# Kernel optimization log

Hardware: AMD Instinct MI355X
Metric: run time of the kernel (lower is better)

Reference implementation:

```python
import jax, jax.numpy as jnp
import numpy as np

N, E, NNZ = 50000, 10000, 250000   # nodes, hyperedges, incidences
IN_CH, H, D = 128, 64, 6           # in_channels, MLP_hidden, stalk dim
EPS = 1e-5


def setup_inputs() -> dict:
    key = jax.random.key(0)
    ks = jax.random.split(key, 12)
    inp = {}
    inp["x"] = jax.random.normal(ks[0], (N, IN_CH), jnp.float32)
    inp["hyperedge_attr"] = jax.random.normal(ks[1], (E, IN_CH), jnp.float32)  # init_hedge='rand'
    inp["node_idx"] = jax.random.randint(ks[2], (NNZ,), 0, N)
    inp["edge_idx"] = jax.random.randint(ks[3], (NNZ,), 0, E)
    inp["node_types"] = jax.random.randint(ks[4], (N,), 0, 3)
    inp["hyperedge_types"] = jax.random.randint(ks[5], (E,), 0, 6)
    s = 1.0 / np.sqrt(IN_CH)
    inp["W_lin"] = jax.random.uniform(ks[6], (IN_CH, H * D), jnp.float32, -s, s)
    inp["b_lin"] = jnp.zeros((H * D,), jnp.float32)
    inp["ln_g"] = jnp.ones((2 * H,), jnp.float32)
    inp["ln_b"] = jnp.zeros((2 * H,), jnp.float32)
    s2 = 1.0 / np.sqrt(2 * H)
    inp["W_sheaf"] = jax.random.uniform(ks[7], (2 * H, D), jnp.float32, -s2, s2)
    inp["b_sheaf"] = jnp.zeros((D,), jnp.float32)
    s3 = 1.0 / np.sqrt(H)
    inp["W_conv0"] = jax.random.uniform(ks[8], (H, H), jnp.float32, -s3, s3)
    inp["b_conv0"] = jnp.zeros((H,), jnp.float32)
    inp["W_conv1"] = jax.random.uniform(ks[9], (H, H), jnp.float32, -s3, s3)
    inp["b_conv1"] = jnp.zeros((H,), jnp.float32)
    return inp


def _layernorm(x, g, b):
    mu = x.mean(-1, keepdims=True)
    var = ((x - mu) ** 2).mean(-1, keepdims=True)
    return (x - mu) * jax.lax.rsqrt(var + EPS) * g + b


def reference(x, hyperedge_attr, node_idx, edge_idx, node_types, hyperedge_types,
              W_lin, b_lin, ln_g, ln_b, W_sheaf, b_sheaf,
              W_conv0, b_conv0, W_conv1, b_conv1):
    # --- input projection + stalk reshape (self.lin) ---
    xs = (x @ W_lin + b_lin).reshape(N * D, H)              # [N*d, H]
    es = (hyperedge_attr @ W_lin + b_lin).reshape(E * D, H)  # [E*d, H]

    # --- SheafBuilderDiag (local_concat, sigmoid act) ---
    xa = xs.reshape(N, D, H).mean(1)   # [N, H] stalk-averaged node feats
    ea = es.reshape(E, D, H).mean(1)   # [E, H]
    feat = jnp.concatenate([xa[node_idx], ea[edge_idx]], axis=-1)  # [NNZ, 2H]
    alpha = jax.nn.sigmoid(_layernorm(feat, ln_g, ln_b) @ W_sheaf + b_sheaf)  # [NNZ, D]

    dr = jnp.arange(D)
    row_exp = (node_idx[:, None] * D + dr).reshape(-1)  # [NNZ*D] expanded node index
    col_exp = (edge_idx[:, None] * D + dr).reshape(-1)  # [NNZ*D] expanded hyperedge index
    a = alpha.reshape(-1)                               # [NNZ*D]

    # --- degree_norm: D^-1 (nodes) and B^-1 (hyperedges) from incidence counts ---
    ones = jnp.ones_like(a)
    Dn = jax.ops.segment_sum(ones, row_exp, num_segments=N * D)
    Dinv = jnp.where(Dn > 0, 1.0 / Dn, 0.0)
    Bn = jax.ops.segment_sum(ones, col_exp, num_segments=E * D)
    Binv = jnp.where(Bn > 0, 1.0 / Bn, 0.0)

    def conv(xin, W, bias):
        # HyperDiffusionDiagSheafConv: out = xW - D^-1 H^T B^-1 H (xW) + bias
        xl = xin @ W
        m = Binv[:, None] * jax.ops.segment_sum(a[:, None] * xl[row_exp], col_exp, num_segments=E * D)
        agg = Dinv[:, None] * jax.ops.segment_sum(a[:, None] * m[col_exp], row_exp, num_segments=N * D)
        return xl - agg + bias

    h1 = jax.nn.elu(conv(xs, W_conv0, b_conv0))   # dropout inactive (eval)
    h2 = conv(h1, W_conv1, b_conv1)
    return jax.nn.elu(h2.reshape(N, H * D))
```

## Files before the change

kernel.cpp:

```cpp
#include <hip/hip_runtime.h>
#include <hip/hip_bf16.h>

#define N_NODES 50000
#define N_EDGES 10000
#define NNZV    250000
#define IN_CH   128
#define HDIM    64
#define DSTALK  6
#define HD      384
#define NROWS   (N_NODES * DSTALK)
#define EROWS   (N_EDGES * DSTALK)

__global__ __launch_bounds__(256) void k_wefft(
    const float* __restrict__ W_lin, const float* __restrict__ W0,
    float* __restrict__ W0effT) {
  int idx = blockIdx.x * blockDim.x + threadIdx.x;
  if (idx >= IN_CH * HD) return;
  int k = idx / HD, j = idx - k * HD;
  int r = j >> 6, h = j & 63;
  float s = 0.f;
#pragma unroll 8
  for (int m = 0; m < HDIM; m++)
    s += W_lin[k * HD + r * HDIM + m] * W0[m * HDIM + h];
  W0effT[(size_t)j * IN_CH + k] = s;
}

#define WS_BASE (IN_CH * HDIM + HD + HDIM)
#define WS_END  (WS_BASE + 780 + HDIM * HDIM)
__global__ __launch_bounds__(256) void k_wsmall(
    const float* __restrict__ W_lin, const float* __restrict__ b_lin,
    const float* __restrict__ W0, const float* __restrict__ W1,
    const float* __restrict__ g, const float* __restrict__ bln,
    const float* __restrict__ Ws, const float* __restrict__ bs,
    float* __restrict__ Wm, float* __restrict__ cm, float* __restrict__ c0,
    float* __restrict__ gwN, float* __restrict__ gwE,
    float* __restrict__ G, float* __restrict__ K, float* __restrict__ W1T) {
  int idx = blockIdx.x * blockDim.x + threadIdx.x;
  if (idx < IN_CH * HDIM) {
    int k = idx >> 6, h = idx & 63;
    float s = 0.f;
#pragma unroll
    for (int r = 0; r < DSTALK; r++) s += W_lin[k * HD + r * HDIM + h];
    Wm[idx] = s * (1.f / 6.f);
  } else if (idx < IN_CH * HDIM + HD) {
    int j = idx - IN_CH * HDIM;
    int r = j >> 6, h = j & 63;
    float s = 0.f;
#pragma unroll 8
    for (int m = 0; m < HDIM; m++) s += b_lin[r * HDIM + m] * W0[m * HDIM + h];
    c0[j] = s;
  } else if (idx < WS_BASE) {
    int h = idx - IN_CH * HDIM - HD;
    float s = 0.f;
#pragma unroll
    for (int r = 0; r < DSTALK; r++) s += b_lin[r * HDIM + h];
    cm[h] = s * (1.f / 6.f);
  } else if (idx < WS_BASE + 384) {
    int i = idx - WS_BASE;
    int h = i / 6, r = i - h * 6;
    gwN[i] = g[h] * Ws[h * DSTALK + r];
  } else if (idx < WS_BASE + 768) {
    int i = idx - WS_BASE - 384;
    int h = i / 6, r = i - h * 6;
    gwE[i] = g[64 + h] * Ws[(64 + h) * DSTALK + r];
  } else if (idx < WS_BASE + 774) {
    int r = idx - WS_BASE - 768;
    float s = 0.f;
    for (int i = 0; i < 2 * HDIM; i++) s += g[i] * Ws[i * DSTALK + r];
    G[r] = s;
  } else if (idx < WS_BASE + 780) {
    int r = idx - WS_BASE - 774;
    float s = 0.f;
    for (int i = 0; i < 2 * HDIM; i++) s += bln[i] * Ws[i * DSTALK + r];
    K[r] = s + bs[r];
  } else if (idx < WS_END) {
    int i = idx - WS_BASE - 780;
    int c = i >> 6, k = i & 63;
    W1T[c * HDIM + k] = W1[k * HDIM + c];
  }
}

__global__ __launch_bounds__(256) void k_xa_stats(
    const float* __restrict__ x, const float* __restrict__ ea,
    const float* __restrict__ Wm, const float* __restrict__ cm,
    const float* __restrict__ gwN, const float* __restrict__ gwE,
    float* __restrict__ stats) {
  __shared__ float lx[64][IN_CH];
  __shared__ float ox[64][HDIM + 1];
  __shared__ float lgw[2][64 * DSTALK];
  const int row0 = blockIdx.x * 64;
  const int tid = threadIdx.x;
  for (int i = tid; i < 2 * 64 * DSTALK; i += 256) {
    int which = i / 384, k = i - which * 384;
    lgw[which][k] = which ? gwE[k] : gwN[k];
  }
  for (int i = tid; i < 64 * IN_CH; i += 256) {
    int r = i >> 7, k = i & 127;
    int row = row0 + r;
    float v = 0.f;
    if (row < N_NODES) v = x[row * IN_CH + k];
    else if (row < N_NODES + N_EDGES) v = ea[(row - N_NODES) * IN_CH + k];
    lx[r][k] = v;
  }
  __syncthreads();
  const int col = tid & 63, rg = tid >> 6;
  float acc[16];
#pragma unroll
  for (int i = 0; i < 16; i++) acc[i] = 0.f;
  for (int k = 0; k < IN_CH; k++) {
    float w = Wm[k * HDIM + col];
#pragma unroll
    for (int i = 0; i < 16; i++) acc[i] += lx[rg * 16 + i][k] * w;
  }
  const float c = cm[col];
#pragma unroll
  for (int i = 0; i < 16; i++) ox[rg * 16 + i][col] = acc[i] + c;
  __syncthreads();
  for (int t = tid; t < 512; t += 256) {
    int row = t >> 3, st = t & 7;
    int grow = row0 + row;
    if (grow >= N_NODES + N_EDGES) continue;
    const float* __restrict__ gw = (grow >= N_NODES) ? lgw[1] : lgw[0];
    float s = 0.f;
    if (st == 0) {
#pragma unroll 8
      for (int h = 0; h < HDIM; h++) s += ox[row][h];
    } else if (st == 1) {
#pragma unroll 8
      for (int h = 0; h < HDIM; h++) { float v = ox[row][h]; s += v * v; }
    } else {
      int r = st - 2;
#pragma unroll 8
      for (int h = 0; h < HDIM; h++) s += ox[row][h] * gw[h * DSTALK + r];
    }
    stats[(size_t)grow * 8 + st] = s;
  }
}

__global__ __launch_bounds__(256, 2) void k_xl0(
    const float* __restrict__ x, const float* __restrict__ W0effT,
    const float* __restrict__ c0, float* __restrict__ xl0) {
  __shared__ float4 aS[8][129];
  __shared__ float4 bS[8][129];
  const int tid = threadIdx.x;
  const int row0 = blockIdx.x * 128;
  const int col0 = blockIdx.y * 128;
  const int tc = tid & 15, tr = tid >> 4;
  float acc[8][8];
#pragma unroll
  for (int i = 0; i < 8; i++)
#pragma unroll
    for (int j = 0; j < 8; j++) acc[i][j] = 0.f;

#pragma unroll 1
  for (int kc = 0; kc < 4; kc++) {
    if (kc) __syncthreads();
#pragma unroll
    for (int i = 0; i < 4; i++) {
      int fidx = tid + (i << 8);
      int kq = fidx & 7, row = fidx >> 3;
      int gk = kc * 32 + kq * 4;
      int grow = row0 + row;
      aS[kq][row] = (grow < N_NODES)
                        ? *(const float4*)(x + (size_t)grow * IN_CH + gk)
                        : make_float4(0.f, 0.f, 0.f, 0.f);
    }
#pragma unroll
    for (int i = 0; i < 4; i++) {
      int fidx = tid + (i << 8);
      int kq = fidx & 7, col = fidx >> 3;
      int gk = kc * 32 + kq * 4;
      bS[kq][col] =
          *(const float4*)(W0effT + (size_t)(col0 + col) * IN_CH + gk);
    }
    __syncthreads();
#pragma unroll 1
    for (int kq = 0; kq < 8; kq++) {
      float4 b[8];
#pragma unroll
      for (int j = 0; j < 8; j++) b[j] = bS[kq][tc + (j << 4)];
#pragma unroll
      for (int i = 0; i < 8; i++) {
        float4 a = aS[kq][tr + (i << 4)];
#pragma unroll
        for (int j = 0; j < 8; j++)
          acc[i][j] += a.x * b[j].x + a.y * b[j].y + a.z * b[j].z + a.w * b[j].w;
      }
    }
  }

  float cc[8];
#pragma unroll
  for (int j = 0; j < 8; j++) cc[j] = c0[col0 + tc + (j << 4)];
#pragma unroll
  for (int i = 0; i < 8; i++) {
    int row = row0 + tr + (i << 4);
    if (row >= N_NODES) continue;
    float* __restrict__ orow = xl0 + (size_t)row * HD + col0;
#pragma unroll
    for (int j = 0; j < 8; j++) {
      orow[tc + (j << 4)] = acc[i][j] + cc[j];
    }
  }
}

__global__ __launch_bounds__(256) void k_xw(
    const float* __restrict__ xin, const float* __restrict__ W1T,
    float* __restrict__ xl) {
  __shared__ float4 aS[8][129];
  __shared__ float4 bS[8][65];
  const int tid = threadIdx.x;
  const int row0 = blockIdx.x * 128;
  const int tc = tid & 15, tr = tid >> 4;
  float acc[8][4];
#pragma unroll
  for (int i = 0; i < 8; i++)
#pragma unroll
    for (int j = 0; j < 4; j++) acc[i][j] = 0.f;

#pragma unroll 1
  for (int kc = 0; kc < 2; kc++) {
    if (kc) __syncthreads();
#pragma unroll
    for (int i = 0; i < 4; i++) {
      int fidx = tid + (i << 8);
      int kq = fidx & 7, row = fidx >> 3;
      int gk = kc * 32 + kq * 4;
      int grow = row0 + row;
      aS[kq][row] = (grow < NROWS)
                        ? *(const float4*)(xin + (size_t)grow * HDIM + gk)
                        : make_float4(0.f, 0.f, 0.f, 0.f);
    }
#pragma unroll
    for (int i = 0; i < 2; i++) {
      int fidx = tid + (i << 8);
      int kq = fidx & 7, col = fidx >> 3;
      int gk = kc * 32 + kq * 4;
      bS[kq][col] = *(const float4*)(W1T + col * HDIM + gk);
    }
    __syncthreads();
#pragma unroll 1
    for (int kq = 0; kq < 8; kq++) {
      float4 b[4];
#pragma unroll
      for (int j = 0; j < 4; j++) b[j] = bS[kq][tc + (j << 4)];
#pragma unroll
      for (int i = 0; i < 8; i++) {
        float4 a = aS[kq][tr + (i << 4)];
#pragma unroll
        for (int j = 0; j < 4; j++)
          acc[i][j] += a.x * b[j].x + a.y * b[j].y + a.z * b[j].z + a.w * b[j].w;
      }
    }
  }
#pragma unroll
  for (int i = 0; i < 8; i++) {
    int row = row0 + tr + (i << 4);
    if (row >= NROWS) continue;
#pragma unroll
    for (int j = 0; j < 4; j++) {
      int col = tc + (j << 4);
      xl[(size_t)row * HDIM + col] = acc[i][j];
    }
  }
}

__global__ __launch_bounds__(256) void k_gather_ex(
    const int* __restrict__ rowE, const int* __restrict__ jlE,
    const int* __restrict__ nlE, const float* __restrict__ alpha,
    const float* __restrict__ x, const float* __restrict__ Binv,
    float* __restrict__ ax) {
  int e = (blockIdx.x * blockDim.x + threadIdx.x) >> 6;
  int lane = threadIdx.x & 63;
  if (e >= N_EDGES) return;
  float acc0[DSTALK], acc1[DSTALK];
#pragma unroll
  for (int r = 0; r < DSTALK; r++) { acc0[r] = 0.f; acc1[r] = 0.f; }
  const int lo = rowE[e], hi = rowE[e + 1];
  int p = lo;
  for (; p + 1 < hi; p += 2) {
    const int j0 = jlE[p],     n0 = nlE[p];
    const int j1 = jlE[p + 1], n1 = nlE[p + 1];
    const float* __restrict__ xr0 = x + (size_t)n0 * IN_CH;
    const float* __restrict__ xr1 = x + (size_t)n1 * IN_CH;
    const float* __restrict__ ar0 = alpha + (size_t)j0 * DSTALK;
    const float* __restrict__ ar1 = alpha + (size_t)j1 * DSTALK;
    float x0a = xr0[lane], x0b = xr0[64 + lane];
    float x1a = xr1[lane], x1b = xr1[64 + lane];
    float a0[DSTALK], a1[DSTALK];
#pragma unroll
    for (int r = 0; r < DSTALK; r++) { a0[r] = ar0[r]; a1[r] = ar1[r]; }
#pragma unroll
    for (int r = 0; r < DSTALK; r++) {
      acc0[r] += a0[r] * x0a + a1[r] * x1a;
      acc1[r] += a0[r] * x0b + a1[r] * x1b;
    }
  }
  if (p < hi) {
    const int j0 = jlE[p], n0 = nlE[p];
    const float* __restrict__ xr0 = x + (size_t)n0 * IN_CH;
    const float* __restrict__ ar0 = alpha + (size_t)j0 * DSTALK;
    float x0a = xr0[lane], x0b = xr0[64 + lane];
#pragma unroll
    for (int r = 0; r < DSTALK; r++) {
      acc0[r] += ar0[r] * x0a;
      acc1[r] += ar0[r] * x0b;
    }
  }
  const float bv = Binv[e];
  float* __restrict__ axe = ax + (size_t)e * (DSTALK * IN_CH);
#pragma unroll
  for (int r = 0; r < DSTALK; r++) {
    axe[r * IN_CH + lane]      = acc0[r] * bv;
    axe[r * IN_CH + 64 + lane] = acc1[r] * bv;
  }
}

__global__ __launch_bounds__(256) void k_edge_gemm(
    const float* __restrict__ ax, const float* __restrict__ W0effT,
    float* __restrict__ msum) {
  __shared__ float4 aS[8][129];
  __shared__ float4 bS[8][65];
  const int tid = threadIdx.x;
  const int e0 = blockIdx.x * 128;
  const int r  = blockIdx.y;
  const int tc = tid & 15, tr = tid >> 4;
  float acc[8][4];
#pragma unroll
  for (int i = 0; i < 8; i++)
#pragma unroll
    for (int j = 0; j < 4; j++) acc[i][j] = 0.f;

#pragma unroll 1
  for (int kc = 0; kc < 4; kc++) {
    if (kc) __syncthreads();
#pragma unroll
    for (int i = 0; i < 4; i++) {
      int fidx = tid + (i << 8);
      int kq = fidx & 7, row = fidx >> 3;
      int gk = kc * 32 + kq * 4;
      int ge = e0 + row;
      aS[kq][row] = (ge < N_EDGES)
          ? *(const float4*)(ax + ((size_t)ge * DSTALK + r) * IN_CH + gk)
          : make_float4(0.f, 0.f, 0.f, 0.f);
    }
#pragma unroll
    for (int i = 0; i < 2; i++) {
      int fidx = tid + (i << 8);
      int kq = fidx & 7, col = fidx >> 3;
      int gk = kc * 32 + kq * 4;
      bS[kq][col] =
          *(const float4*)(W0effT + (size_t)(r * 64 + col) * IN_CH + gk);
    }
    __syncthreads();
#pragma unroll 1
    for (int kq = 0; kq < 8; kq++) {
      float4 b[4];
#pragma unroll
      for (int j = 0; j < 4; j++) b[j] = bS[kq][tc + (j << 4)];
#pragma unroll
      for (int i = 0; i < 8; i++) {
        float4 a = aS[kq][tr + (i << 4)];
#pragma unroll
        for (int j = 0; j < 4; j++)
          acc[i][j] += a.x * b[j].x + a.y * b[j].y + a.z * b[j].z + a.w * b[j].w;
      }
    }
  }
#pragma unroll
  for (int i = 0; i < 8; i++) {
    int ge = e0 + tr + (i << 4);
    if (ge >= N_EDGES) continue;
    float* __restrict__ mrow = msum + (size_t)ge * HD + r * 64;
#pragma unroll
    for (int j = 0; j < 4; j++) {
      mrow[tc + (j << 4)] = acc[i][j];
    }
  }
}

__global__ __launch_bounds__(256) void k_sheaf2(
    const int* __restrict__ nidx, const int* __restrict__ eidx,
    const float* __restrict__ stats,
    const float* __restrict__ G, const float* __restrict__ K,
    float* __restrict__ alpha) {
  int j = blockIdx.x * blockDim.x + threadIdx.x;
  if (j >= NNZV) return;
  int n = nidx[j], e = eidx[j];
  const float4* __restrict__ sn = (const float4*)(stats + (size_t)n * 8);
  const float4* __restrict__ se = (const float4*)(stats + ((size_t)(N_NODES + e)) * 8);
  float4 a0 = sn[0], a1 = sn[1];
  float4 b0 = se[0], b1 = se[1];
  float mu = (a0.x + b0.x) * (1.f / 128.f);
  float var = (a0.y + b0.y) * (1.f / 128.f) - mu * mu;
  float rs = rsqrtf(var + 1e-5f);
  float p[DSTALK] = {a0.z + b0.z, a0.w + b0.w, a1.x + b1.x,
                     a1.y + b1.y, a1.z + b1.z, a1.w + b1.w};
#pragma unroll
  for (int r = 0; r < DSTALK; r++) {
    float z = rs * (p[r] - mu * G[r]) + K[r];
    alpha[(size_t)j * DSTALK + r] = 1.f / (1.f + expf(-z));
  }
}

__global__ void k_count(const int* __restrict__ nidx, const int* __restrict__ eidx,
                        int* __restrict__ cntN, int* __restrict__ cntE) {
  int j = blockIdx.x * blockDim.x + threadIdx.x;
  if (j < NNZV) {
    atomicAdd(&cntN[nidx[j]], 1);
    atomicAdd(&cntE[eidx[j]], 1);
  }
}

__global__ __launch_bounds__(256) void k_scan_a(
    const int* __restrict__ cnt, int n, int* __restrict__ row,
    int* __restrict__ bsum) {
  const int b = blockIdx.x, t = threadIdx.x;
  const int i0 = b * 512 + 2 * t, i1 = i0 + 1;
  int c0 = (i0 < n) ? cnt[i0] : 0;
  int c1 = (i1 < n) ? cnt[i1] : 0;
  int ts = c0 + c1;
  const int lane = t & 63, wv = t >> 6;
  int s = ts;
#pragma unroll
  for (int o = 1; o < 64; o <<= 1) {
    int v = __shfl_up(s, o);
    if (lane >= o) s += v;
  }
  __shared__ int wsum[4];
  if (lane == 63) wsum[wv] = s;
  __syncthreads();
  int wbase = 0;
#pragma unroll
  for (int wprev = 0; wprev < 3; wprev++)
    if (wprev < wv) wbase += wsum[wprev];
  const int incl = wbase + s;
  const int excl = incl - ts;
  if (i0 < n) row[i0] = excl;
  if (i1 < n) row[i1] = excl + c0;
  if (t == 255) bsum[b] = incl;
}

__global__ __launch_bounds__(128) void k_scan_b(
    const int* __restrict__ bsum, int nb, int* __restrict__ bbase) {
  const int t = threadIdx.x;
  int v = (t < nb) ? bsum[t] : 0;
  const int lane = t & 63, wv = t >> 6;
  int s = v;
#pragma unroll
  for (int o = 1; o < 64; o <<= 1) {
    int u = __shfl_up(s, o);
    if (lane >= o) s += u;
  }
  __shared__ int wsum[2];
  if (lane == 63) wsum[wv] = s;
  __syncthreads();
  const int incl = ((wv == 1) ? wsum[0] : 0) + s;
  if (t < nb) bbase[t] = incl - v;
  if (t == 127) bbase[nb] = incl;
}

__global__ __launch_bounds__(256) void k_scan_c(
    const int* __restrict__ cnt, const int* __restrict__ bbase, int n, int nb,
    int* __restrict__ row, int* __restrict__ fill, float* __restrict__ inv) {
  int i = blockIdx.x * blockDim.x + threadIdx.x;
  if (i < n) {
    int v = row[i] + bbase[i >> 9];
    row[i] = v;
    fill[i] = v;
    int c = cnt[i];
    inv[i] = c > 0 ? 1.f / (float)c : 0.f;
  }
  if (i == 0) row[n] = bbase[nb];
}

__global__ void k_fill(const int* __restrict__ nidx, const int* __restrict__ eidx,
                       int* __restrict__ fillN, int* __restrict__ fillE,
                       int* __restrict__ jlN, int* __restrict__ jlE,
                       int* __restrict__ elN, int* __restrict__ nlE) {
  int j = blockIdx.x * blockDim.x + threadIdx.x;
  if (j < NNZV) {
    int n = nidx[j], e = eidx[j];
    int p = atomicAdd(&fillN[n], 1);
    jlN[p] = j; elN[p] = e;
    int q = atomicAdd(&fillE[e], 1);
    jlE[q] = j; nlE[q] = n;
  }
}

__global__ __launch_bounds__(256) void k_gather_e(
    const int* __restrict__ rowE, const int* __restrict__ jlE,
    const int* __restrict__ nlE, const float* __restrict__ alpha,
    const float* __restrict__ xl, const float* __restrict__ Binv,
    float* __restrict__ msum) {
  int e = (blockIdx.x * blockDim.x + threadIdx.x) >> 6;
  int lane = threadIdx.x & 63;
  if (e >= N_EDGES) return;
  float acc[DSTALK];
#pragma unroll
  for (int r = 0; r < DSTALK; r++) acc[r] = 0.f;
  const int lo = rowE[e], hi = rowE[e + 1];
  int p = lo;
  for (; p + 3 < hi; p += 4) {
    int jj[4], nn[4];
#pragma unroll
    for (int u = 0; u < 4; u++) { jj[u] = jlE[p + u]; nn[u] = nlE[p + u]; }
    float v[4][DSTALK], a[4][DSTALK];
#pragma unroll
    for (int u = 0; u < 4; u++) {
      const float* __restrict__ xr = xl + (size_t)nn[u] * HD + lane;
      const float* __restrict__ ar = alpha + (size_t)jj[u] * DSTALK;
#pragma unroll
      for (int r = 0; r < DSTALK; r++) { v[u][r] = xr[r * HDIM]; a[u][r] = ar[r]; }
    }
#pragma unroll
    for (int r = 0; r < DSTALK; r++)
      acc[r] += a[0][r] * v[0][r] + a[1][r] * v[1][r] +
                a[2][r] * v[2][r] + a[3][r] * v[3][r];
  }
  for (; p < hi; p++) {
    const int j0 = jlE[p], n0 = nlE[p];
    const float* __restrict__ xr0 = xl + (size_t)n0 * HD + lane;
    const float* __restrict__ ar0 = alpha + (size_t)j0 * DSTALK;
#pragma unroll
    for (int r = 0; r < DSTALK; r++) acc[r] += ar0[r] * xr0[r * HDIM];
  }
  const float bv = Binv[e];
  float* __restrict__ mr = msum + (size_t)e * HD + lane;
#pragma unroll
  for (int r = 0; r < DSTALK; r++) mr[r * HDIM] = acc[r] * bv;
}

__global__ __launch_bounds__(256) void k_gather_n(
    const int* __restrict__ rowN, const int* __restrict__ jlN,
    const int* __restrict__ elN, const float* __restrict__ alpha,
    const float* __restrict__ msum, const float* __restrict__ Dinv,
    const float* __restrict__ xl, const float* __restrict__ bias,
    float* __restrict__ outp) {
  int n = (blockIdx.x * blockDim.x + threadIdx.x) >> 6;
  int lane = threadIdx.x & 63;
  if (n >= N_NODES) return;
  float acc[DSTALK];
#pragma unroll
  for (int r = 0; r < DSTALK; r++) acc[r] = 0.f;
  const int lo = rowN[n], hi = rowN[n + 1];
  int p = lo;
  for (; p + 3 < hi; p += 4) {
    int jj[4], ee[4];
#pragma unroll
    for (int u = 0; u < 4; u++) { jj[u] = jlN[p + u]; ee[u] = elN[p + u]; }
    float v[4][DSTALK], a[4][DSTALK];
#pragma unroll
    for (int u = 0; u < 4; u++) {
      const float* __restrict__ mr = msum + (size_t)ee[u] * HD + lane;
      const float* __restrict__ ar = alpha + (size_t)jj[u] * DSTALK;
#pragma unroll
      for (int r = 0; r < DSTALK; r++) { v[u][r] = mr[r * HDIM]; a[u][r] = ar[r]; }
    }
#pragma unroll
    for (int r = 0; r < DSTALK; r++)
      acc[r] += a[0][r] * v[0][r] + a[1][r] * v[1][r] +
                a[2][r] * v[2][r] + a[3][r] * v[3][r];
  }
  for (; p < hi; p++) {
    const int j0 = jlN[p], e0 = elN[p];
    const float* __restrict__ mr0 = msum + (size_t)e0 * HD + lane;
    const float* __restrict__ ar0 = alpha + (size_t)j0 * DSTALK;
#pragma unroll
    for (int r = 0; r < DSTALK; r++) acc[r] += ar0[r] * mr0[r * HDIM];
  }
  const float dv = Dinv[n];
  const float bb = bias[lane];
  const float* __restrict__ xr = xl + (size_t)n * HD + lane;
  float* __restrict__ orow = outp + (size_t)n * HD + lane;
#pragma unroll
  for (int r = 0; r < DSTALK; r++) {
    float v = xr[r * HDIM] + bb - dv * acc[r];
    orow[r * HDIM] = v > 0.f ? v : expm1f(v);
  }
}

extern "C" void kernel_launch(void* const* d_in, const int* in_sizes, int n_in,
                              void* d_out, int out_size, void* d_ws, size_t ws_size,
                              hipStream_t stream) {
  const float* x    = (const float*)d_in[0];
  const float* hea  = (const float*)d_in[1];
  const int*  nidx  = (const int*)d_in[2];
  const int*  eidx  = (const int*)d_in[3];
  const float* W_lin = (const float*)d_in[6];
  const float* b_lin = (const float*)d_in[7];
  const float* ln_g  = (const float*)d_in[8];
  const float* ln_b  = (const float*)d_in[9];
  const float* W_sh  = (const float*)d_in[10];
  const float* b_sh  = (const float*)d_in[11];
  const float* W_c0  = (const float*)d_in[12];
  const float* b_c0  = (const float*)d_in[13];
  const float* W_c1  = (const float*)d_in[14];
  const float* b_c1  = (const float*)d_in[15];
  float* out = (float*)d_out;

  char* ws = (char*)d_ws;
  size_t off = 0;
  auto alloc = [&](size_t bytes) {
    size_t o = off;
    off = (off + bytes + 255) & ~(size_t)255;
    return o;
  };
  size_t o_xl0   = alloc((size_t)NROWS * HDIM * 4);
  size_t o_msum  = alloc((size_t)EROWS * HDIM * 4);
  size_t o_alpha = alloc((size_t)NNZV * DSTALK * 4);
  size_t o_stats = alloc((size_t)(N_NODES + N_EDGES) * 8 * 4);
  size_t o_jlN   = alloc((size_t)NNZV * 4);
  size_t o_jlE   = alloc((size_t)NNZV * 4);
  size_t o_elN   = alloc((size_t)NNZV * 4);
  size_t o_nlE   = alloc((size_t)NNZV * 4);
  size_t o_cntN  = alloc((size_t)N_NODES * 4);
  size_t o_cntE  = alloc((size_t)N_EDGES * 4);
  size_t o_rowN  = alloc((size_t)(N_NODES + 1) * 4);
  size_t o_rowE  = alloc((size_t)(N_EDGES + 1) * 4);
  size_t o_filN  = alloc((size_t)N_NODES * 4);
  size_t o_filE  = alloc((size_t)N_EDGES * 4);
  size_t o_Dinv  = alloc((size_t)N_NODES * 4);
  size_t o_Binv  = alloc((size_t)N_EDGES * 4);
  size_t o_bsN   = alloc((size_t)256 * 4);
  size_t o_bbN   = alloc((size_t)256 * 4);
  size_t o_bsE   = alloc((size_t)256 * 4);
  size_t o_bbE   = alloc((size_t)256 * 4);
  size_t o_WeffT = alloc((size_t)IN_CH * HD * 4);
  size_t o_Wm    = alloc((size_t)IN_CH * HDIM * 4);
  size_t o_cm    = alloc((size_t)HDIM * 4);
  size_t o_c0    = alloc((size_t)HD * 4);
  size_t o_gwN   = alloc((size_t)64 * DSTALK * 4);
  size_t o_gwE   = alloc((size_t)64 * DSTALK * 4);
  size_t o_G     = alloc((size_t)DSTALK * 4);
  size_t o_K     = alloc((size_t)DSTALK * 4);
  size_t o_W1T   = alloc((size_t)HDIM * HDIM * 4);

  float* xl0    = (float*)(ws + o_xl0);
  float* msum   = (float*)(ws + o_msum);
  float* alpha  = (float*)(ws + o_alpha);
  float* stats  = (float*)(ws + o_stats);
  int*   jlN    = (int*)(ws + o_jlN);
  int*   jlE    = (int*)(ws + o_jlE);
  int*   elN    = (int*)(ws + o_elN);
  int*   nlE    = (int*)(ws + o_nlE);
  int*   cntN   = (int*)(ws + o_cntN);
  int*   cntE   = (int*)(ws + o_cntE);
  int*   rowN   = (int*)(ws + o_rowN);
  int*   rowE   = (int*)(ws + o_rowE);
  int*   filN   = (int*)(ws + o_filN);
  int*   filE   = (int*)(ws + o_filE);
  float* Dinv   = (float*)(ws + o_Dinv);
  float* Binv   = (float*)(ws + o_Binv);
  int*   bsN    = (int*)(ws + o_bsN);
  int*   bbN    = (int*)(ws + o_bbN);
  int*   bsE    = (int*)(ws + o_bsE);
  int*   bbE    = (int*)(ws + o_bbE);
  float* W0effT = (float*)(ws + o_WeffT);
  float* Wm     = (float*)(ws + o_Wm);
  float* cm     = (float*)(ws + o_cm);
  float* c0     = (float*)(ws + o_c0);
  float* gwN    = (float*)(ws + o_gwN);
  float* gwE    = (float*)(ws + o_gwE);
  float* G      = (float*)(ws + o_G);
  float* K      = (float*)(ws + o_K);
  float* W1T    = (float*)(ws + o_W1T);

  float* ax = (float*)d_out;

  const int NB_N = (N_NODES + 511) / 512;
  const int NB_E = (N_EDGES + 511) / 512;

  k_wefft<<<(IN_CH * HD + 255) / 256, 256, 0, stream>>>(W_lin, W_c0, W0effT);
  k_wsmall<<<(WS_END + 255) / 256, 256, 0, stream>>>(
      W_lin, b_lin, W_c0, W_c1, ln_g, ln_b, W_sh, b_sh,
      Wm, cm, c0, gwN, gwE, G, K, W1T);

  hipMemsetAsync(ws + o_cntN, 0, (size_t)N_NODES * 4, stream);
  hipMemsetAsync(ws + o_cntE, 0, (size_t)N_EDGES * 4, stream);
  k_count<<<(NNZV + 255) / 256, 256, 0, stream>>>(nidx, eidx, cntN, cntE);
  k_scan_a<<<NB_N, 256, 0, stream>>>(cntN, N_NODES, rowN, bsN);
  k_scan_a<<<NB_E, 256, 0, stream>>>(cntE, N_EDGES, rowE, bsE);
  k_scan_b<<<1, 128, 0, stream>>>(bsN, NB_N, bbN);
  k_scan_b<<<1, 128, 0, stream>>>(bsE, NB_E, bbE);
  k_scan_c<<<(N_NODES + 255) / 256, 256, 0, stream>>>(cntN, bbN, N_NODES, NB_N,
                                                      rowN, filN, Dinv);
  k_scan_c<<<(N_EDGES + 255) / 256, 256, 0, stream>>>(cntE, bbE, N_EDGES, NB_E,
                                                      rowE, filE, Binv);
  k_fill<<<(NNZV + 255) / 256, 256, 0, stream>>>(nidx, eidx, filN, filE,
                                                 jlN, jlE, elN, nlE);

  k_xa_stats<<<(N_NODES + N_EDGES + 63) / 64, 256, 0, stream>>>(
      x, hea, Wm, cm, gwN, gwE, stats);

  k_sheaf2<<<(NNZV + 255) / 256, 256, 0, stream>>>(nidx, eidx, stats, G, K, alpha);

  k_gather_ex<<<(N_EDGES + 3) / 4, 256, 0, stream>>>(rowE, jlE, nlE, alpha, x,
                                                     Binv, ax);
  {
    dim3 ge((N_EDGES + 127) / 128, DSTALK);
    k_edge_gemm<<<ge, 256, 0, stream>>>(ax, W0effT, msum);
  }
  {
    dim3 g((N_NODES + 127) / 128, HD / 128);
    k_xl0<<<g, 256, 0, stream>>>(x, W0effT, c0, xl0);
  }
  k_gather_n<<<(N_NODES + 3) / 4, 256, 0, stream>>>(rowN, jlN, elN, alpha, msum, Dinv,
                                                    xl0, b_c0, xl0);

  k_xw<<<(NROWS + 127) / 128, 256, 0, stream>>>(xl0, W1T, xl0);
  k_gather_e<<<(N_EDGES + 3) / 4, 256, 0, stream>>>(rowE, jlE, nlE, alpha, xl0, Binv, msum);
  k_gather_n<<<(N_NODES + 3) / 4, 256, 0, stream>>>(rowN, jlN, elN, alpha, msum, Dinv,
                                                    xl0, b_c1, out);

  (void)in_sizes; (void)n_in; (void)out_size; (void)ws_size;
}
```

Measured before the change: 652.6 us.

## Compute node projection GEMM with split-bf16 MFMA instead of FP32 FMA

Adds a kernel that splits x and the effective weight into high and low bf16 parts, and rewrites k_xl0 to use 16x16x32 bf16 MFMA with three products (hi*hi, hi*lo, lo*hi) to emulate near-fp32 accuracy. This moves the largest dense GEMM off the vector FMA units onto matrix cores. The cost is an extra pass over x (read fp32, write two bf16 copies), staged in spare space of the output buffer, plus slightly lower precision than true fp32.

Result: faster. 626.8 us (-4.0%).

```diff
diff --git a/kernel.cpp b/kernel.cpp
--- a/kernel.cpp
+++ b/kernel.cpp
@@ -10,6 +10,9 @@
 #define HD      384
 #define NROWS   (N_NODES * DSTALK)
 #define EROWS   (N_EDGES * DSTALK)
+
+typedef __attribute__((ext_vector_type(8))) short bf16x8;
+typedef __attribute__((ext_vector_type(4))) float f32x4;
 
 __global__ __launch_bounds__(256) void k_wefft(
     const float* __restrict__ W_lin, const float* __restrict__ W0,
@@ -80,6 +83,28 @@
   }
 }
 
+__global__ __launch_bounds__(256) void k_split(
+    const float* __restrict__ src, int n4,
+    unsigned short* __restrict__ hi, unsigned short* __restrict__ lo) {
+  int i = blockIdx.x * blockDim.x + threadIdx.x;
+  if (i >= n4) return;
+  float4 v = ((const float4*)src)[i];
+  float f[4] = {v.x, v.y, v.z, v.w};
+  unsigned short h[4], l[4];
+#pragma unroll
+  for (int u = 0; u < 4; u++) {
+    unsigned int b = __float_as_uint(f[u]);
+    unsigned int r = (b + 0x7FFFu + ((b >> 16) & 1u)) >> 16;
+    h[u] = (unsigned short)r;
+    float d = f[u] - __uint_as_float(r << 16);
+    unsigned int b2 = __float_as_uint(d);
+    unsigned int r2 = (b2 + 0x7FFFu + ((b2 >> 16) & 1u)) >> 16;
+    l[u] = (unsigned short)r2;
+  }
+  ((ushort4*)hi)[i] = make_ushort4(h[0], h[1], h[2], h[3]);
+  ((ushort4*)lo)[i] = make_ushort4(l[0], l[1], l[2], l[3]);
+}
+
 __global__ __launch_bounds__(256) void k_xa_stats(
     const float* __restrict__ x, const float* __restrict__ ea,
     const float* __restrict__ Wm, const float* __restrict__ cm,
@@ -138,68 +163,69 @@
 }
 
 __global__ __launch_bounds__(256, 2) void k_xl0(
-    const float* __restrict__ x, const float* __restrict__ W0effT,
+    const unsigned short* __restrict__ xh, const unsigned short* __restrict__ xl,
+    const unsigned short* __restrict__ wh, const unsigned short* __restrict__ wl,
     const float* __restrict__ c0, float* __restrict__ xl0) {
-  __shared__ float4 aS[8][129];
-  __shared__ float4 bS[8][129];
+  __shared__ bf16x8 aH[4][132], aL[4][132], bH[4][132], bL[4][132];
   const int tid = threadIdx.x;
   const int row0 = blockIdx.x * 128;
   const int col0 = blockIdx.y * 128;
-  const int tc = tid & 15, tr = tid >> 4;
-  float acc[8][8];
-#pragma unroll
-  for (int i = 0; i < 8; i++)
-#pragma unroll
-    for (int j = 0; j < 8; j++) acc[i][j] = 0.f;
+  const int lane = tid & 63, wv = tid >> 6;
+  const int wrow = wv * 32;
+  const int kg = lane >> 4, rr = lane & 15;
+  f32x4 acc[2][8];
+#pragma unroll
+  for (int i = 0; i < 2; i++)
+#pragma unroll
+    for (int j = 0; j < 8; j++) acc[i][j] = (f32x4){0.f, 0.f, 0.f, 0.f};
 
 #pragma unroll 1
-  for (int kc = 0; kc < 4; kc++) {
-    if (kc) __syncthreads();
-#pragma unroll
-    for (int i = 0; i < 4; i++) {
-      int fidx = tid + (i << 8);
-      int kq = fidx & 7, row = fidx >> 3;
-      int gk = kc * 32 + kq * 4;
-      int grow = row0 + row;
-      aS[kq][row] = (grow < N_NODES)
-                        ? *(const float4*)(x + (size_t)grow * IN_CH + gk)
-                        : make_float4(0.f, 0.f, 0.f, 0.f);
-    }
-#pragma unroll
-    for (int i = 0; i < 4; i++) {
-      int fidx = tid + (i << 8);
-      int kq = fidx & 7, col = fidx >> 3;
-      int gk = kc * 32 + kq * 4;
-      bS[kq][col] =
-          *(const float4*)(W0effT + (size_t)(col0 + col) * IN_CH + gk);
+  for (int ks = 0; ks < 4; ks++) {
+    if (ks) __syncthreads();
+    const int kbase = ks * 32;
+#pragma unroll
+    for (int i = 0; i < 2; i++) {
+      int f2 = tid + (i << 8);
+      int g = f2 & 3, rc = f2 >> 2;
+      bf16x8 zv = {0, 0, 0, 0, 0, 0, 0, 0};
+      int grow = row0 + rc;
+      const size_t soff = (size_t)grow * IN_CH + kbase + g * 8;
+      bool ok = (grow < N_NODES);
+      aH[g][rc] = ok ? *(const bf16x8*)(xh + soff) : zv;
+      aL[g][rc] = ok ? *(const bf16x8*)(xl + soff) : zv;
+      const size_t woff = (size_t)(col0 + rc) * IN_CH + kbase + g * 8;
+      bH[g][rc] = *(const bf16x8*)(wh + woff);
+      bL[g][rc] = *(const bf16x8*)(wl + woff);
     }
     __syncthreads();
-#pragma unroll 1
-    for (int kq = 0; kq < 8; kq++) {
-      float4 b[8];
-#pragma unroll
-      for (int j = 0; j < 8; j++) b[j] = bS[kq][tc + (j << 4)];
-#pragma unroll
-      for (int i = 0; i < 8; i++) {
-        float4 a = aS[kq][tr + (i << 4)];
-#pragma unroll
-        for (int j = 0; j < 8; j++)
-          acc[i][j] += a.x * b[j].x + a.y * b[j].y + a.z * b[j].z + a.w * b[j].w;
+    bf16x8 a0h = aH[kg][wrow + rr];
+    bf16x8 a0l = aL[kg][wrow + rr];
+    bf16x8 a1h = aH[kg][wrow + 16 + rr];
+    bf16x8 a1l = aL[kg][wrow + 16 + rr];
+#pragma unroll
+    for (int cb = 0; cb < 8; cb++) {
+      bf16x8 vbh = bH[kg][cb * 16 + rr];
+      bf16x8 vbl = bL[kg][cb * 16 + rr];
+      acc[0][cb] = __builtin_amdgcn_mfma_f32_16x16x32_bf16(a0h, vbh, acc[0][cb], 0, 0, 0);
+      acc[0][cb] = __builtin_amdgcn_mfma_f32_16x16x32_bf16(a0h, vbl, acc[0][cb], 0, 0, 0);
+      acc[0][cb] = __builtin_amdgcn_mfma_f32_16x16x32_bf16(a0l, vbh, acc[0][cb], 0, 0, 0);
+      acc[1][cb] = __builtin_amdgcn_mfma_f32_16x16x32_bf16(a1h, vbh, acc[1][cb], 0, 0, 0);
+      acc[1][cb] = __builtin_amdgcn_mfma_f32_16x16x32_bf16(a1h, vbl, acc[1][cb], 0, 0, 0);
+      acc[1][cb] = __builtin_amdgcn_mfma_f32_16x16x32_bf16(a1l, vbh, acc[1][cb], 0, 0, 0);
+    }
+  }
+
+#pragma unroll
+  for (int cb = 0; cb < 8; cb++) {
+    float cc = c0[col0 + cb * 16 + rr];
+#pragma unroll
+    for (int rb = 0; rb < 2; rb++) {
+#pragma unroll
+      for (int r = 0; r < 4; r++) {
+        int row = row0 + wrow + rb * 16 + kg * 4 + r;
+        if (row < N_NODES)
+          xl0[(size_t)row * HD + col0 + cb * 16 + rr] = acc[rb][cb][r] + cc;
       }
-    }
-  }
-
-  float cc[8];
-#pragma unroll
-  for (int j = 0; j < 8; j++) cc[j] = c0[col0 + tc + (j << 4)];
-#pragma unroll
-  for (int i = 0; i < 8; i++) {
-    int row = row0 + tr + (i << 4);
-    if (row >= N_NODES) continue;
-    float* __restrict__ orow = xl0 + (size_t)row * HD + col0;
-#pragma unroll
-    for (int j = 0; j < 8; j++) {
-      orow[tc + (j << 4)] = acc[i][j] + cc[j];
     }
   }
 }
@@ -667,6 +693,10 @@
   float* W1T    = (float*)(ws + o_W1T);
 
   float* ax = (float*)d_out;
+  unsigned short* xh  = (unsigned short*)((char*)d_out + ((size_t)32 << 20));
+  unsigned short* xlo = (unsigned short*)((char*)d_out + ((size_t)48 << 20));
+  unsigned short* wh  = (unsigned short*)((char*)d_out + ((size_t)64 << 20));
+  unsigned short* wl  = (unsigned short*)((char*)d_out + ((size_t)66 << 20));
 
   const int NB_N = (N_NODES + 511) / 512;
   const int NB_E = (N_EDGES + 511) / 512;
@@ -675,6 +705,10 @@
   k_wsmall<<<(WS_END + 255) / 256, 256, 0, stream>>>(
       W_lin, b_lin, W_c0, W_c1, ln_g, ln_b, W_sh, b_sh,
       Wm, cm, c0, gwN, gwE, G, K, W1T);
+  k_split<<<((N_NODES * IN_CH / 4) + 255) / 256, 256, 0, stream>>>(
+      x, N_NODES * IN_CH / 4, xh, xlo);
+  k_split<<<((HD * IN_CH / 4) + 255) / 256, 256, 0, stream>>>(
+      W0effT, HD * IN_CH / 4, wh, wl);
 
   hipMemsetAsync(ws + o_cntN, 0, (size_t)N_NODES * 4, stream);
   hipMemsetAsync(ws + o_cntE, 0, (size_t)N_EDGES * 4, stream);
@@ -703,7 +737,7 @@
   }
   {
     dim3 g((N_NODES + 127) / 128, HD / 128);
-    k_xl0<<<g, 256, 0, stream>>>(x, W0effT, c0, xl0);
+    k_xl0<<<g, 256, 0, stream>>>(xh, xlo, wh, wl, c0, xl0);
   }
   k_gather_n<<<(N_NODES + 3) / 4, 256, 0, stream>>>(rowN, jlN, elN, alpha, msum, Dinv,
                                                     xl0, b_c0, xl0);
```
